# Performance work log

Hardware: AMD Instinct MI355X
Metric: run time of the kernel (lower is better)

Reference implementation:

```python
import jax, jax.numpy as jnp
import numpy as np

C_EM, H_EM, C_A = 256, 8, 32
S, R = 1024, 256
LN_EPS = 1e-5
MASK_BIAS = 1e9


def setup_inputs() -> dict:
    key = jax.random.key(0)
    ks = jax.random.split(key, 8)
    sc = 0.02
    m = jax.random.normal(ks[0], (S, R, C_EM), jnp.float32)
    # binary column mask (float mask in the original; int here so it is a constant)
    mask = (jax.random.uniform(ks[1], (S, R)) < 0.9).astype(jnp.int32)
    return {
        "m": m,
        "ln_g": jnp.ones((C_EM,), jnp.float32),
        "ln_b": jnp.zeros((C_EM,), jnp.float32),
        "w_q": jax.random.normal(ks[2], (C_EM, H_EM, C_A), jnp.float32) * sc,
        "w_k": jax.random.normal(ks[3], (C_EM, C_A), jnp.float32) * sc,
        "w_v": jax.random.normal(ks[4], (C_EM, C_A), jnp.float32) * sc,
        "w_g": jax.random.normal(ks[5], (C_EM, H_EM, C_A), jnp.float32) * sc,
        "b_g": jnp.zeros((H_EM, C_A), jnp.float32),
        "w_o": jax.random.normal(ks[6], (H_EM, C_A, C_EM), jnp.float32) * sc,
        "b_o": jnp.zeros((C_EM,), jnp.float32),
        "mask": mask,
    }


def reference(m, ln_g, ln_b, w_q, w_k, w_v, w_g, b_g, w_o, b_o, mask):
    maskf = mask.astype(m.dtype)  # [s, r]
    # LayerNorm over c_em (biased variance, eps=1e-5, torch default)
    mu = jnp.mean(m, axis=-1, keepdims=True)
    var = jnp.mean((m - mu) ** 2, axis=-1, keepdims=True)
    x = (m - mu) * jax.lax.rsqrt(var + LN_EPS) * ln_g + ln_b  # [s, r, c]
    # masked mean-pool over s -> per-column query
    q_pool = jnp.sum(x * maskf[..., None], axis=-3) / (jnp.sum(maskf, axis=-2)[..., None] + 1e-10)  # [r, c]
    Q = jnp.einsum('rc,chd->rhd', q_pool, w_q) * (1.0 / np.sqrt(C_A))  # [r, h, d]
    K = jnp.einsum('src,cd->srd', x, w_k)  # [s, r, d]
    V = jnp.einsum('src,cd->srd', x, w_v)  # [s, r, d]
    G = jax.nn.sigmoid(jnp.einsum('src,chd->srhd', x, w_g) + b_g)  # [s, r, h, d]
    bias = (maskf - 1.0) * MASK_BIAS  # [s, r]
    logits = jnp.einsum('rhd,srd->srh', Q, K) + bias[..., None]  # [s, r, h]
    A = jax.nn.softmax(logits, axis=-3)  # softmax over s
    O = jnp.einsum('srh,srd->rhd', A, V)  # [r, h, d]
    out = jnp.einsum('srhd,hdc->src', O[None, :, :, :] * G, w_o) + b_o  # [s, r, c]
    return out
```

## Files before the change

### kernel.cpp

```cpp
#include <hip/hip_runtime.h>
#include <math.h>

#define S_DIM 1024
#define R_DIM 256
#define C_DIM 256
#define SCALE 0.17677669529663687f

typedef short bf16x8 __attribute__((ext_vector_type(8)));
typedef float f32x4 __attribute__((ext_vector_type(4)));

__device__ __forceinline__ float wred(float v) {
#pragma unroll
  for (int m = 32; m >= 1; m >>= 1) v += __shfl_xor(v, m, 64);
  return v;
}

__device__ __forceinline__ short f2bf(float f) {
  union { float f; unsigned u; } v;
  v.f = f;
  unsigned r = v.u + 0x7fffu + ((v.u >> 16) & 1u);
  return (short)(r >> 16);
}

__device__ __forceinline__ float bf2f(short s) {
  union { unsigned u; float f; } v;
  v.u = ((unsigned)(unsigned short)s) << 16;
  return v.f;
}

__device__ __forceinline__ float fast_sigmoid_mul(float o, float gl) {
  return o * __builtin_amdgcn_rcpf(1.f + __expf(-gl));
}

__global__ __launch_bounds__(256)
void k0_prep(const float* __restrict__ w_g, const float* __restrict__ w_o,
             const float* __restrict__ w_k, const float* __restrict__ w_v,
             short* __restrict__ wgB, short* __restrict__ woB,
             short* __restrict__ wkvB) {
  const int id = blockIdx.x * 256 + threadIdx.x;
  if (id < 16384) {
    const int which = id >> 13;
    const int s = id & 8191;
    const int n = s & 255, g = (s >> 8) & 3, kb = s >> 10;
    const float* W = which ? w_o : w_g;
    short* Out = which ? woB : wgB;
#pragma unroll
    for (int j = 0; j < 8; ++j)
      Out[(((size_t)kb * 256 + n) * 4 + g) * 8 + j] =
          f2bf(W[(size_t)(kb * 32 + g * 8 + j) * 256 + n]);
  } else {
    const int s = id - 16384;
    const int n = s & 63, g = (s >> 6) & 3, kb = s >> 8;
    const float* W = (n < 32) ? w_k : w_v;
    const int nn = n & 31;
#pragma unroll
    for (int j = 0; j < 8; ++j)
      wkvB[(((size_t)kb * 64 + n) * 4 + g) * 8 + j] =
          f2bf(W[(size_t)(kb * 32 + g * 8 + j) * 32 + nn]);
  }
}

__global__ __launch_bounds__(256, 3)
void k1_ln_kv(const float* __restrict__ mIn, const float* __restrict__ ln_g,
              const float* __restrict__ ln_b, const short* __restrict__ wkvB,
              const int* __restrict__ mask,
              float* __restrict__ mu_ws, float* __restrict__ rs_ws,
              float* __restrict__ K_ws, float* __restrict__ V_ws,
              float* __restrict__ pool_ws) {
  __shared__ __align__(16) short A_lds[2048 * 8];
  __shared__ float mask_s[64];
  __shared__ float4 poolp[4][64];
  const int r  = blockIdx.y;
  const int s0 = blockIdx.x * 64;
  const int t  = threadIdx.x;

  if (t < 64) mask_s[t] = mask[(s0 + t) * R_DIM + r] ? 1.f : 0.f;

  {
    const int rw = t >> 2;
    const int q  = t & 3;
    const size_t p = (size_t)(s0 + rw) * R_DIM + r;
    const float* src = mIn + p * C_DIM + q * 64;
    float4 xv[16];
    float sum = 0.f, ssq = 0.f;
#pragma unroll
    for (int i = 0; i < 16; ++i) {
      xv[i] = *(const float4*)(src + i * 4);
      sum += xv[i].x + xv[i].y + xv[i].z + xv[i].w;
      ssq += xv[i].x * xv[i].x + xv[i].y * xv[i].y + xv[i].z * xv[i].z +
             xv[i].w * xv[i].w;
    }
    sum += __shfl_xor(sum, 1, 64); ssq += __shfl_xor(ssq, 1, 64);
    sum += __shfl_xor(sum, 2, 64); ssq += __shfl_xor(ssq, 2, 64);
    const float mu = sum * (1.f / 256.f);
    const float var = ssq * (1.f / 256.f) - mu * mu;
    const float rs = rsqrtf(var + 1e-5f);
    if (q == 0) { mu_ws[p] = mu; rs_ws[p] = rs; }

    const int gw = rw >> 4;
    const int lf0 = rw & 15;
#pragma unroll
    for (int kh = 0; kh < 2; ++kh) {
      const int kb = 2 * q + kh;
#pragma unroll
      for (int g = 0; g < 4; ++g) {
        const int lidx = kh * 32 + g * 8;
        const float4 a0 = xv[lidx >> 2], a1 = xv[(lidx >> 2) + 1];
        const float4 g0 = *(const float4*)(ln_g + kb * 32 + g * 8);
        const float4 g1 = *(const float4*)(ln_g + kb * 32 + g * 8 + 4);
        const float4 b0 = *(const float4*)(ln_b + kb * 32 + g * 8);
        const float4 b1 = *(const float4*)(ln_b + kb * 32 + g * 8 + 4);
        bf16x8 f;
        f[0] = f2bf((a0.x - mu) * rs * g0.x + b0.x);
        f[1] = f2bf((a0.y - mu) * rs * g0.y + b0.y);
        f[2] = f2bf((a0.z - mu) * rs * g0.z + b0.z);
        f[3] = f2bf((a0.w - mu) * rs * g0.w + b0.w);
        f[4] = f2bf((a1.x - mu) * rs * g1.x + b1.x);
        f[5] = f2bf((a1.y - mu) * rs * g1.y + b1.y);
        f[6] = f2bf((a1.z - mu) * rs * g1.z + b1.z);
        f[7] = f2bf((a1.w - mu) * rs * g1.w + b1.w);
        int byte = (((gw * 8 + kb) * 64 + lf0 + g * 16) << 4) ^ (((kb >> 1) & 3) << 5);
        *(bf16x8*)((char*)A_lds + byte) = f;
      }
    }
  }
  __syncthreads();

  {
    const int w = t >> 6, l = t & 63;
    const int lm = l & 15, g = l >> 4;
    f32x4 acc[4];
#pragma unroll
    for (int ni = 0; ni < 4; ++ni) acc[ni] = (f32x4){0.f, 0.f, 0.f, 0.f};
#pragma unroll
    for (int kb = 0; kb < 8; ++kb) {
      const int byte = (((w * 8 + kb) * 64 + l) << 4) ^ (((kb >> 1) & 3) << 5);
      const bf16x8 a = *(const bf16x8*)((char*)A_lds + byte);
      bf16x8 bfr[4];
#pragma unroll
      for (int ni = 0; ni < 4; ++ni)
        bfr[ni] = *(const bf16x8*)(wkvB + (((size_t)kb * 64 + lm + ni * 16) * 4 + g) * 8);
#pragma unroll
      for (int ni = 0; ni < 4; ++ni)
        acc[ni] = __builtin_amdgcn_mfma_f32_16x16x32_bf16(a, bfr[ni], acc[ni], 0, 0, 0);
    }
#pragma unroll
    for (int ni = 0; ni < 4; ++ni) {
      const int col = lm + ni * 16;
      float* Out = (col < 32) ? K_ws : V_ws;
      const int cc = col & 31;
#pragma unroll
      for (int reg = 0; reg < 4; ++reg) {
        const int s = s0 + w * 16 + g * 4 + reg;
        Out[((size_t)s * R_DIM + r) * 32 + cc] = acc[ni][reg];
      }
    }
  }

  {
    const int lc = t & 63;
    const int wq = t >> 6;
    const int kb = lc >> 3, g2 = (lc >> 1) & 3, bh = (lc & 1) * 4;
    float4 ps = make_float4(0.f, 0.f, 0.f, 0.f);
    for (int i = 0; i < 16; ++i) {
      const int rloc = (i + lc) & 15;
      const int byte =
          ((((wq * 8 + kb) * 64 + rloc + g2 * 16) << 4) + bh * 2) ^ (((kb >> 1) & 3) << 5);
      const short4 xb = *(const short4*)((char*)A_lds + byte);
      const float mk = mask_s[wq * 16 + rloc];
      ps.x += mk * bf2f(xb.x);
      ps.y += mk * bf2f(xb.y);
      ps.z += mk * bf2f(xb.z);
      ps.w += mk * bf2f(xb.w);
    }
    poolp[wq][lc] = ps;
  }
  __syncthreads();
  if (t < 64) {
    const float4 a = poolp[0][t], b = poolp[1][t], c = poolp[2][t], d = poolp[3][t];
    atomicAdd(&pool_ws[r * C_DIM + t * 4 + 0], a.x + b.x + c.x + d.x);
    atomicAdd(&pool_ws[r * C_DIM + t * 4 + 1], a.y + b.y + c.y + d.y);
    atomicAdd(&pool_ws[r * C_DIM + t * 4 + 2], a.z + b.z + c.z + d.z);
    atomicAdd(&pool_ws[r * C_DIM + t * 4 + 3], a.w + b.w + c.w + d.w);
  }
}

__global__ __launch_bounds__(256, 2)
void k3_attn(const float* __restrict__ K_ws, const float* __restrict__ V_ws,
             const int* __restrict__ mask, const float* __restrict__ pool_ws,
             const float* __restrict__ w_q, float* __restrict__ O_ws) {
  __shared__ float q[256];
  __shared__ float qp[256];
  __shared__ float lg[1024 * 9];
  __shared__ float kv[256 * 36];
  __shared__ float mh[8], inv[8];
  __shared__ float wsum[4];
  const int r = blockIdx.x, t = threadIdx.x;

  int mk[4];
#pragma unroll
  for (int ch = 0; ch < 4; ++ch) mk[ch] = mask[(ch * 256 + t) * R_DIM + r];
  float cf = wred((float)(mk[0] + mk[1] + mk[2] + mk[3]));
  if ((t & 63) == 0) wsum[t >> 6] = cf;
  __syncthreads();
  const float denom = wsum[0] + wsum[1] + wsum[2] + wsum[3] + 1e-10f;
  qp[t] = pool_ws[r * C_DIM + t] / denom;
  __syncthreads();
  {
    float qa = 0.f;
    for (int c = 0; c < 256; ++c) qa += qp[c] * w_q[c * 256 + t];
    q[t] = qa * SCALE;
  }
  __syncthreads();

  for (int ch = 0; ch < 4; ++ch) {
    const int sb = ch * 256;
    __syncthreads();
    for (int f = t; f < 2048; f += 256) {
      const int sl = f >> 3, dq = f & 7;
      *(float4*)(kv + sl * 36 + dq * 4) =
          *(const float4*)(K_ws + ((size_t)(sb + sl) * R_DIM + r) * 32 + dq * 4);
    }
    __syncthreads();
    float kr[32];
#pragma unroll
    for (int dq = 0; dq < 8; ++dq)
      *(float4*)(kr + dq * 4) = *(float4*)(kv + t * 36 + dq * 4);
    const float bias = mk[ch] ? 0.f : -1e9f;
#pragma unroll
    for (int h = 0; h < 8; ++h) {
      float a = 0.f;
#pragma unroll
      for (int d = 0; d < 32; ++d) a += q[h * 32 + d] * kr[d];
      lg[(sb + t) * 9 + h] = a + bias;
    }
  }
  __syncthreads();
  {
    const int h = t >> 5, l32 = t & 31;
    float mx = -INFINITY;
    for (int k = 0; k < 32; ++k) mx = fmaxf(mx, lg[(l32 + 32 * k) * 9 + h]);
#pragma unroll
    for (int mkk = 16; mkk >= 1; mkk >>= 1) mx = fmaxf(mx, __shfl_xor(mx, mkk, 64));
    float sm = 0.f;
    for (int k = 0; k < 32; ++k) sm += __expf(lg[(l32 + 32 * k) * 9 + h] - mx);
#pragma unroll
    for (int mkk = 16; mkk >= 1; mkk >>= 1) sm += __shfl_xor(sm, mkk, 64);
    if (l32 == 0) { mh[h] = mx; inv[h] = 1.f / sm; }
  }
  __syncthreads();
  for (int f = t; f < 8192; f += 256) {
    const int s = f >> 3, h = f & 7;
    lg[s * 9 + h] = __expf(lg[s * 9 + h] - mh[h]) * inv[h];
  }
  const int h = t >> 5, d = t & 31;
  float o = 0.f;
  for (int ch = 0; ch < 4; ++ch) {
    const int sb = ch * 256;
    __syncthreads();
    for (int f = t; f < 2048; f += 256) {
      const int sl = f >> 3, dq = f & 7;
      *(float4*)(kv + sl * 36 + dq * 4) =
          *(const float4*)(V_ws + ((size_t)(sb + sl) * R_DIM + r) * 32 + dq * 4);
    }
    __syncthreads();
    for (int sl = 0; sl < 256; ++sl)
      o += lg[(sb + sl) * 9 + h] * kv[sl * 36 + d];
  }
  O_ws[r * 256 + t] = o;
}

__global__ __launch_bounds__(256, 4)
void k4_mfma(const float* __restrict__ mIn, const float* __restrict__ ln_g,
             const float* __restrict__ ln_b, const float* __restrict__ mu_ws,
             const float* __restrict__ rs_ws, const short* __restrict__ wgB,
             const float* __restrict__ b_g, const float* __restrict__ O_ws,
             const short* __restrict__ woB, const float* __restrict__ b_o,
             float* __restrict__ out) {
  __shared__ __align__(16) short A_lds[2048 * 8];
  const int t = threadIdx.x;
  const int p0 = blockIdx.x * 64;
  const int r0 = p0 & 255;
  const int l = t & 63;
  const int w = t >> 6;
  const int lm = l & 15;
  const int g = l >> 4;
  const int col = w * 64 + lm;

  bf16x8 bb_c[4], bb_n[4];
#pragma unroll
  for (int ni = 0; ni < 4; ++ni)
    bb_c[ni] = *(const bf16x8*)(wgB + (((size_t)0 * 256 + col + ni * 16) * 4 + g) * 8);

  {
    const int row = w * 16 + lm;
    const size_t p = (size_t)(p0 + row);
    const float mu = mu_ws[p], rs = rs_ws[p];
    const float* mrow = mIn + p * 256 + g * 8;
    const float* gp = ln_g + g * 8;
    const float* bp = ln_b + g * 8;
#pragma unroll
    for (int kb = 0; kb < 8; ++kb) {
      const float4 m0 = *(const float4*)(mrow + kb * 32);
      const float4 m1 = *(const float4*)(mrow + kb * 32 + 4);
      const float4 g0 = *(const float4*)(gp + kb * 32);
      const float4 g1 = *(const float4*)(gp + kb * 32 + 4);
      const float4 b0 = *(const float4*)(bp + kb * 32);
      const float4 b1 = *(const float4*)(bp + kb * 32 + 4);
      bf16x8 xf;
      xf[0] = f2bf((m0.x - mu) * rs * g0.x + b0.x);
      xf[1] = f2bf((m0.y - mu) * rs * g0.y + b0.y);
      xf[2] = f2bf((m0.z - mu) * rs * g0.z + b0.z);
      xf[3] = f2bf((m0.w - mu) * rs * g0.w + b0.w);
      xf[4] = f2bf((m1.x - mu) * rs * g1.x + b1.x);
      xf[5] = f2bf((m1.y - mu) * rs * g1.y + b1.y);
      xf[6] = f2bf((m1.z - mu) * rs * g1.z + b1.z);
      xf[7] = f2bf((m1.w - mu) * rs * g1.w + b1.w);
      *(bf16x8*)(A_lds + ((w * 8 + kb) * 64 + l) * 8) = xf;
    }
  }
  __syncthreads();

  f32x4 acc[4][4];

#pragma unroll
  for (int ni = 0; ni < 4; ++ni) {
    const float bg = b_g[col + ni * 16];
#pragma unroll
    for (int mi = 0; mi < 4; ++mi) acc[mi][ni] = (f32x4){bg, bg, bg, bg};
  }
#pragma unroll
  for (int kb = 0; kb < 8; ++kb) {
    bf16x8 a[4];
#pragma unroll
    for (int mi = 0; mi < 4; ++mi)
      a[mi] = *(const bf16x8*)(A_lds + ((mi * 8 + kb) * 64 + l) * 8);
    if (kb < 7) {
#pragma unroll
      for (int ni = 0; ni < 4; ++ni)
        bb_n[ni] = *(const bf16x8*)(wgB +
            (((size_t)(kb + 1) * 256 + col + ni * 16) * 4 + g) * 8);
    }
#pragma unroll
    for (int mi = 0; mi < 4; ++mi)
#pragma unroll
      for (int ni = 0; ni < 4; ++ni)
        acc[mi][ni] = __builtin_amdgcn_mfma_f32_16x16x32_bf16(a[mi], bb_c[ni], acc[mi][ni], 0, 0, 0);
#pragma unroll
    for (int ni = 0; ni < 4; ++ni) bb_c[ni] = bb_n[ni];
  }

#pragma unroll
  for (int ni = 0; ni < 4; ++ni)
    bb_c[ni] = *(const bf16x8*)(woB + (((size_t)0 * 256 + col + ni * 16) * 4 + g) * 8);
  __syncthreads();

#pragma unroll
  for (int mi = 0; mi < 4; ++mi) {
#pragma unroll
    for (int ni = 0; ni < 4; ++ni) {
      const int c2 = col + ni * 16;
      const int kb2 = c2 >> 5, g2 = (c2 >> 3) & 3, b2 = c2 & 7;
#pragma unroll
      for (int reg = 0; reg < 4; ++reg) {
        const int row = mi * 16 + g * 4 + reg;
        const float o = O_ws[(r0 + row) * 256 + c2];
        const float tv = fast_sigmoid_mul(o, acc[mi][ni][reg]);
        const int u = (mi * 8 + kb2) * 64 + (g * 4 + reg) + g2 * 16;
        const int byte = ((u << 4) ^ (((u >> 4) & 3) << 4)) + b2 * 2;
        *(short*)((char*)A_lds + byte) = f2bf(tv);
      }
    }
  }
  __syncthreads();

#pragma unroll
  for (int ni = 0; ni < 4; ++ni) {
    const float bo = b_o[col + ni * 16];
#pragma unroll
    for (int mi = 0; mi < 4; ++mi) acc[mi][ni] = (f32x4){bo, bo, bo, bo};
  }
#pragma unroll
  for (int kb = 0; kb < 8; ++kb) {
    bf16x8 a[4];
#pragma unroll
    for (int mi = 0; mi < 4; ++mi) {
      const int u = (mi * 8 + kb) * 64 + l;
      a[mi] = *(const bf16x8*)((char*)A_lds + ((u << 4) ^ (g << 4)));
    }
    if (kb < 7) {
#pragma unroll
      for (int ni = 0; ni < 4; ++ni)
        bb_n[ni] = *(const bf16x8*)(woB +
            (((size_t)(kb + 1) * 256 + col + ni * 16) * 4 + g) * 8);
    }
#pragma unroll
    for (int mi = 0; mi < 4; ++mi)
#pragma unroll
      for (int ni = 0; ni < 4; ++ni)
        acc[mi][ni] = __builtin_amdgcn_mfma_f32_16x16x32_bf16(a[mi], bb_c[ni], acc[mi][ni], 0, 0, 0);
#pragma unroll
    for (int ni = 0; ni < 4; ++ni) bb_c[ni] = bb_n[ni];
  }

#pragma unroll
  for (int mi = 0; mi < 4; ++mi)
#pragma unroll
    for (int ni = 0; ni < 4; ++ni)
#pragma unroll
      for (int reg = 0; reg < 4; ++reg) {
        const int row = mi * 16 + g * 4 + reg;
        out[(size_t)(p0 + row) * 256 + col + ni * 16] = acc[mi][ni][reg];
      }
}

extern "C" void kernel_launch(void* const* d_in, const int* in_sizes, int n_in,
                              void* d_out, int out_size, void* d_ws, size_t ws_size,
                              hipStream_t stream) {
  const float* mIn  = (const float*)d_in[0];
  const float* ln_g = (const float*)d_in[1];
  const float* ln_b = (const float*)d_in[2];
  const float* w_q  = (const float*)d_in[3];
  const float* w_k  = (const float*)d_in[4];
  const float* w_v  = (const float*)d_in[5];
  const float* w_g  = (const float*)d_in[6];
  const float* b_g  = (const float*)d_in[7];
  const float* w_o  = (const float*)d_in[8];
  const float* b_o  = (const float*)d_in[9];
  const int*   mask = (const int*)d_in[10];
  float* outp = (float*)d_out;

  char* ws = (char*)d_ws;
  const size_t NP = (size_t)S_DIM * R_DIM;
  float* mu_ws   = (float*)ws;
  float* rs_ws   = mu_ws + NP;
  float* K_ws    = rs_ws + NP;
  float* V_ws    = K_ws + NP * 32;
  float* pool_ws = V_ws + NP * 32;
  float* O_ws    = pool_ws + 65536;
  short* wgB     = (short*)(O_ws + 65536);
  short* woB     = wgB + 65536;
  short* wkvB    = woB + 65536;

  hipMemsetAsync(pool_ws, 0, 65536 * sizeof(float), stream);

  k0_prep<<<72, 256, 0, stream>>>(w_g, w_o, w_k, w_v, wgB, woB, wkvB);
  k1_ln_kv<<<dim3(S_DIM / 64, R_DIM), 256, 0, stream>>>(
      mIn, ln_g, ln_b, wkvB, mask, mu_ws, rs_ws, K_ws, V_ws, pool_ws);
  k3_attn<<<R_DIM, 256, 0, stream>>>(K_ws, V_ws, mask, pool_ws, w_q, O_ws);
  k4_mfma<<<dim3(S_DIM * R_DIM / 64), 256, 0, stream>>>(
      mIn, ln_g, ln_b, mu_ws, rs_ws, wgB, b_g, O_ws, woB, b_o, outp);
}
```

Before: 395.9 us.

## Process two 64-row tiles per block with double-buffered LDS software pipeline

The final fused gate/output GEMM kernel now handles two 64-row tiles per block, using two LDS buffers. Loads of the second tile's input rows overlap the first tile's gate GEMM, and the scatter and second GEMM stages of the two tiles are interleaved. This is meant to hide global-load latency and barrier stalls behind MFMA work. In exchange it doubles LDS use, raises register pressure (16 float4 prefetch registers), halves the grid and lowers the occupancy target to 2 blocks per CU. It also drops the previous B-fragment register prefetch.

```diff
diff --git a/kernel.cpp b/kernel.cpp
--- a/kernel.cpp
+++ b/kernel.cpp
@@ -270,148 +270,196 @@
   O_ws[r * 256 + t] = o;
 }
 
-__global__ __launch_bounds__(256, 4)
+#define K4_WRITEX(L, MU, RS)                                                \
+  {                                                                         \
+    const float* gp_ = ln_g + g * 8;                                        \
+    const float* bp_ = ln_b + g * 8;                                        \
+    _Pragma("unroll")                                                       \
+    for (int kb = 0; kb < 8; ++kb) {                                        \
+      const float4 g0 = *(const float4*)(gp_ + kb * 32);                    \
+      const float4 g1 = *(const float4*)(gp_ + kb * 32 + 4);                \
+      const float4 b0 = *(const float4*)(bp_ + kb * 32);                    \
+      const float4 b1 = *(const float4*)(bp_ + kb * 32 + 4);                \
+      const float4 m0 = mv[2 * kb], m1 = mv[2 * kb + 1];                    \
+      bf16x8 xf;                                                            \
+      xf[0] = f2bf((m0.x - (MU)) * (RS) * g0.x + b0.x);                     \
+      xf[1] = f2bf((m0.y - (MU)) * (RS) * g0.y + b0.y);                     \
+      xf[2] = f2bf((m0.z - (MU)) * (RS) * g0.z + b0.z);                     \
+      xf[3] = f2bf((m0.w - (MU)) * (RS) * g0.w + b0.w);                     \
+      xf[4] = f2bf((m1.x - (MU)) * (RS) * g1.x + b1.x);                     \
+      xf[5] = f2bf((m1.y - (MU)) * (RS) * g1.y + b1.y);                     \
+      xf[6] = f2bf((m1.z - (MU)) * (RS) * g1.z + b1.z);                     \
+      xf[7] = f2bf((m1.w - (MU)) * (RS) * g1.w + b1.w);                     \
+      *(bf16x8*)((L) + ((w * 8 + kb) * 64 + l) * 8) = xf;                   \
+    }                                                                       \
+  }
+
+#define K4_G1(L)                                                            \
+  {                                                                         \
+    _Pragma("unroll")                                                       \
+    for (int ni = 0; ni < 4; ++ni) {                                        \
+      const float bg = b_g[col + ni * 16];                                  \
+      _Pragma("unroll")                                                     \
+      for (int mi = 0; mi < 4; ++mi) acc[mi][ni] = (f32x4){bg, bg, bg, bg}; \
+    }                                                                       \
+    _Pragma("unroll")                                                       \
+    for (int kb = 0; kb < 8; ++kb) {                                        \
+      bf16x8 bb[4], a[4];                                                   \
+      _Pragma("unroll")                                                     \
+      for (int ni = 0; ni < 4; ++ni)                                        \
+        bb[ni] = *(const bf16x8*)(wgB +                                     \
+            (((size_t)kb * 256 + col + ni * 16) * 4 + g) * 8);              \
+      _Pragma("unroll")                                                     \
+      for (int mi = 0; mi < 4; ++mi)                                        \
+        a[mi] = *(const bf16x8*)((L) + ((mi * 8 + kb) * 64 + l) * 8);       \
+      _Pragma("unroll")                                                     \
+      for (int mi = 0; mi < 4; ++mi)                                        \
+        _Pragma("unroll")                                                   \
+        for (int ni = 0; ni < 4; ++ni)                                      \
+          acc[mi][ni] = __builtin_amdgcn_mfma_f32_16x16x32_bf16(            \
+              a[mi], bb[ni], acc[mi][ni], 0, 0, 0);                         \
+    }                                                                       \
+  }
+
+#define K4_SCAT(L, R0)                                                      \
+  {                                                                         \
+    _Pragma("unroll")                                                       \
+    for (int mi = 0; mi < 4; ++mi) {                                        \
+      _Pragma("unroll")                                                     \
+      for (int ni = 0; ni < 4; ++ni) {                                      \
+        const int c2 = col + ni * 16;                                       \
+        const int kb2 = c2 >> 5, g2 = (c2 >> 3) & 3, b2 = c2 & 7;           \
+        _Pragma("unroll")                                                   \
+        for (int reg = 0; reg < 4; ++reg) {                                 \
+          const int rw2 = mi * 16 + g * 4 + reg;                            \
+          const float o = O_ws[((R0) + rw2) * 256 + c2];                    \
+          const float tv = fast_sigmoid_mul(o, acc[mi][ni][reg]);           \
+          const int u = (mi * 8 + kb2) * 64 + (g * 4 + reg) + g2 * 16;      \
+          const int byte = ((u << 4) ^ (((u >> 4) & 3) << 4)) + b2 * 2;     \
+          *(short*)((char*)(L) + byte) = f2bf(tv);                          \
+        }                                                                   \
+      }                                                                     \
+    }                                                                       \
+  }
+
+#define K4_G2(L)                                                            \
+  {                                                                         \
+    _Pragma("unroll")                                                       \
+    for (int ni = 0; ni < 4; ++ni) {                                        \
+      const float bo = b_o[col + ni * 16];                                  \
+      _Pragma("unroll")                                                     \
+      for (int mi = 0; mi < 4; ++mi) acc[mi][ni] = (f32x4){bo, bo, bo, bo}; \
+    }                                                                       \
+    _Pragma("unroll")                                                       \
+    for (int kb = 0; kb < 8; ++kb) {                                        \
+      bf16x8 bb[4], a[4];                                                   \
+      _Pragma("unroll")                                                     \
+      for (int ni = 0; ni < 4; ++ni)                                        \
+        bb[ni] = *(const bf16x8*)(woB +                                     \
+            (((size_t)kb * 256 + col + ni * 16) * 4 + g) * 8);              \
+      _Pragma("unroll")                                                     \
+      for (int mi = 0; mi < 4; ++mi) {                                      \
+        const int u = (mi * 8 + kb) * 64 + l;                               \
+        a[mi] = *(const bf16x8*)((char*)(L) + ((u << 4) ^ (g << 4)));       \
+      }                                                                     \
+      _Pragma("unroll")                                                     \
+      for (int mi = 0; mi < 4; ++mi)                                        \
+        _Pragma("unroll")                                                   \
+        for (int ni = 0; ni < 4; ++ni)                                      \
+          acc[mi][ni] = __builtin_amdgcn_mfma_f32_16x16x32_bf16(            \
+              a[mi], bb[ni], acc[mi][ni], 0, 0, 0);                         \
+    }                                                                       \
+  }
+
+#define K4_STORE(PBASE)                                                     \
+  _Pragma("unroll")                                                         \
+  for (int mi = 0; mi < 4; ++mi)                                            \
+    _Pragma("unroll")                                                       \
+    for (int ni = 0; ni < 4; ++ni)                                          \
+      _Pragma("unroll")                                                     \
+      for (int reg = 0; reg < 4; ++reg) {                                   \
+        const int rw2 = mi * 16 + g * 4 + reg;                              \
+        out[(size_t)((PBASE) + rw2) * 256 + col + ni * 16] =                \
+            acc[mi][ni][reg];                                               \
+      }
+
+__global__ __launch_bounds__(256, 2)
 void k4_mfma(const float* __restrict__ mIn, const float* __restrict__ ln_g,
              const float* __restrict__ ln_b, const float* __restrict__ mu_ws,
              const float* __restrict__ rs_ws, const short* __restrict__ wgB,
              const float* __restrict__ b_g, const float* __restrict__ O_ws,
              const short* __restrict__ woB, const float* __restrict__ b_o,
              float* __restrict__ out) {
-  __shared__ __align__(16) short A_lds[2048 * 8];
+  __shared__ __align__(16) short L0[2048 * 8];
+  __shared__ __align__(16) short L1[2048 * 8];
   const int t = threadIdx.x;
-  const int p0 = blockIdx.x * 64;
-  const int r0 = p0 & 255;
-  const int l = t & 63;
-  const int w = t >> 6;
-  const int lm = l & 15;
-  const int g = l >> 4;
+  const int l = t & 63, w = t >> 6, lm = l & 15, g = l >> 4;
+  const int pA = blockIdx.x * 128;
+  const int r0A = pA & 255;
+  const int r0B = r0A + 64;
   const int col = w * 64 + lm;
-
-  bf16x8 bb_c[4], bb_n[4];
-#pragma unroll
-  for (int ni = 0; ni < 4; ++ni)
-    bb_c[ni] = *(const bf16x8*)(wgB + (((size_t)0 * 256 + col + ni * 16) * 4 + g) * 8);
-
-  {
-    const int row = w * 16 + lm;
-    const size_t p = (size_t)(p0 + row);
-    const float mu = mu_ws[p], rs = rs_ws[p];
+  const int srow = w * 16 + lm;
+
+  float4 mv[16];
+  f32x4 acc[4][4];
+
+  {
+    const size_t p = (size_t)(pA + srow);
+    const float mu0 = mu_ws[p], rs0 = rs_ws[p];
     const float* mrow = mIn + p * 256 + g * 8;
-    const float* gp = ln_g + g * 8;
-    const float* bp = ln_b + g * 8;
 #pragma unroll
     for (int kb = 0; kb < 8; ++kb) {
-      const float4 m0 = *(const float4*)(mrow + kb * 32);
-      const float4 m1 = *(const float4*)(mrow + kb * 32 + 4);
-      const float4 g0 = *(const float4*)(gp + kb * 32);
-      const float4 g1 = *(const float4*)(gp + kb * 32 + 4);
-      const float4 b0 = *(const float4*)(bp + kb * 32);
-      const float4 b1 = *(const float4*)(bp + kb * 32 + 4);
-      bf16x8 xf;
-      xf[0] = f2bf((m0.x - mu) * rs * g0.x + b0.x);
-      xf[1] = f2bf((m0.y - mu) * rs * g0.y + b0.y);
-      xf[2] = f2bf((m0.z - mu) * rs * g0.z + b0.z);
-      xf[3] = f2bf((m0.w - mu) * rs * g0.w + b0.w);
-      xf[4] = f2bf((m1.x - mu) * rs * g1.x + b1.x);
-      xf[5] = f2bf((m1.y - mu) * rs * g1.y + b1.y);
-      xf[6] = f2bf((m1.z - mu) * rs * g1.z + b1.z);
-      xf[7] = f2bf((m1.w - mu) * rs * g1.w + b1.w);
-      *(bf16x8*)(A_lds + ((w * 8 + kb) * 64 + l) * 8) = xf;
-    }
-  }
-  __syncthreads();
-
-  f32x4 acc[4][4];
-
-#pragma unroll
-  for (int ni = 0; ni < 4; ++ni) {
-    const float bg = b_g[col + ni * 16];
-#pragma unroll
-    for (int mi = 0; mi < 4; ++mi) acc[mi][ni] = (f32x4){bg, bg, bg, bg};
-  }
-#pragma unroll
-  for (int kb = 0; kb < 8; ++kb) {
-    bf16x8 a[4];
-#pragma unroll
-    for (int mi = 0; mi < 4; ++mi)
-      a[mi] = *(const bf16x8*)(A_lds + ((mi * 8 + kb) * 64 + l) * 8);
-    if (kb < 7) {
+      mv[2 * kb]     = *(const float4*)(mrow + kb * 32);
+      mv[2 * kb + 1] = *(const float4*)(mrow + kb * 32 + 4);
+    }
+    K4_WRITEX(L0, mu0, rs0)
+  }
+  __syncthreads();
+
+  {
+    const size_t pB = (size_t)(pA + 64 + srow);
+    const float mu1 = mu_ws[pB], rs1 = rs_ws[pB];
+    const float* mrowB = mIn + pB * 256 + g * 8;
+#pragma unroll
+    for (int ni = 0; ni < 4; ++ni) {
+      const float bg = b_g[col + ni * 16];
+#pragma unroll
+      for (int mi = 0; mi < 4; ++mi) acc[mi][ni] = (f32x4){bg, bg, bg, bg};
+    }
+#pragma unroll
+    for (int kb = 0; kb < 8; ++kb) {
+      bf16x8 bb[4], a[4];
 #pragma unroll
       for (int ni = 0; ni < 4; ++ni)
-        bb_n[ni] = *(const bf16x8*)(wgB +
-            (((size_t)(kb + 1) * 256 + col + ni * 16) * 4 + g) * 8);
-    }
-#pragma unroll
-    for (int mi = 0; mi < 4; ++mi)
-#pragma unroll
-      for (int ni = 0; ni < 4; ++ni)
-        acc[mi][ni] = __builtin_amdgcn_mfma_f32_16x16x32_bf16(a[mi], bb_c[ni], acc[mi][ni], 0, 0, 0);
-#pragma unroll
-    for (int ni = 0; ni < 4; ++ni) bb_c[ni] = bb_n[ni];
-  }
-
-#pragma unroll
-  for (int ni = 0; ni < 4; ++ni)
-    bb_c[ni] = *(const bf16x8*)(woB + (((size_t)0 * 256 + col + ni * 16) * 4 + g) * 8);
-  __syncthreads();
-
-#pragma unroll
-  for (int mi = 0; mi < 4; ++mi) {
-#pragma unroll
-    for (int ni = 0; ni < 4; ++ni) {
-      const int c2 = col + ni * 16;
-      const int kb2 = c2 >> 5, g2 = (c2 >> 3) & 3, b2 = c2 & 7;
-#pragma unroll
-      for (int reg = 0; reg < 4; ++reg) {
-        const int row = mi * 16 + g * 4 + reg;
-        const float o = O_ws[(r0 + row) * 256 + c2];
-        const float tv = fast_sigmoid_mul(o, acc[mi][ni][reg]);
-        const int u = (mi * 8 + kb2) * 64 + (g * 4 + reg) + g2 * 16;
-        const int byte = ((u << 4) ^ (((u >> 4) & 3) << 4)) + b2 * 2;
-        *(short*)((char*)A_lds + byte) = f2bf(tv);
-      }
-    }
-  }
-  __syncthreads();
-
-#pragma unroll
-  for (int ni = 0; ni < 4; ++ni) {
-    const float bo = b_o[col + ni * 16];
-#pragma unroll
-    for (int mi = 0; mi < 4; ++mi) acc[mi][ni] = (f32x4){bo, bo, bo, bo};
-  }
-#pragma unroll
-  for (int kb = 0; kb < 8; ++kb) {
-    bf16x8 a[4];
-#pragma unroll
-    for (int mi = 0; mi < 4; ++mi) {
-      const int u = (mi * 8 + kb) * 64 + l;
-      a[mi] = *(const bf16x8*)((char*)A_lds + ((u << 4) ^ (g << 4)));
-    }
-    if (kb < 7) {
-#pragma unroll
-      for (int ni = 0; ni < 4; ++ni)
-        bb_n[ni] = *(const bf16x8*)(woB +
-            (((size_t)(kb + 1) * 256 + col + ni * 16) * 4 + g) * 8);
-    }
-#pragma unroll
-    for (int mi = 0; mi < 4; ++mi)
-#pragma unroll
-      for (int ni = 0; ni < 4; ++ni)
-        acc[mi][ni] = __builtin_amdgcn_mfma_f32_16x16x32_bf16(a[mi], bb_c[ni], acc[mi][ni], 0, 0, 0);
-#pragma unroll
-    for (int ni = 0; ni < 4; ++ni) bb_c[ni] = bb_n[ni];
-  }
-
-#pragma unroll
-  for (int mi = 0; mi < 4; ++mi)
-#pragma unroll
-    for (int ni = 0; ni < 4; ++ni)
-#pragma unroll
-      for (int reg = 0; reg < 4; ++reg) {
-        const int row = mi * 16 + g * 4 + reg;
-        out[(size_t)(p0 + row) * 256 + col + ni * 16] = acc[mi][ni][reg];
-      }
+        bb[ni] = *(const bf16x8*)(wgB +
+            (((size_t)kb * 256 + col + ni * 16) * 4 + g) * 8);
+      mv[2 * kb]     = *(const float4*)(mrowB + kb * 32);
+      mv[2 * kb + 1] = *(const float4*)(mrowB + kb * 32 + 4);
+#pragma unroll
+      for (int mi = 0; mi < 4; ++mi)
+        a[mi] = *(const bf16x8*)(L0 + ((mi * 8 + kb) * 64 + l) * 8);
+#pragma unroll
+      for (int mi = 0; mi < 4; ++mi)
+#pragma unroll
+        for (int ni = 0; ni < 4; ++ni)
+          acc[mi][ni] = __builtin_amdgcn_mfma_f32_16x16x32_bf16(
+              a[mi], bb[ni], acc[mi][ni], 0, 0, 0);
+    }
+    K4_WRITEX(L1, mu1, rs1)
+  }
+  __syncthreads();
+
+  K4_SCAT(L0, r0A)
+  K4_G1(L1)
+  __syncthreads();
+
+  K4_SCAT(L1, r0B)
+  K4_G2(L0)
+  K4_STORE(pA)
+  __syncthreads();
+
+  K4_G2(L1)
+  K4_STORE(pA + 64)
 }
 
 extern "C" void kernel_launch(void* const* d_in, const int* in_sizes, int n_in,
@@ -448,6 +496,6 @@
   k1_ln_kv<<<dim3(S_DIM / 64, R_DIM), 256, 0, stream>>>(
       mIn, ln_g, ln_b, wkvB, mask, mu_ws, rs_ws, K_ws, V_ws, pool_ws);
   k3_attn<<<R_DIM, 256, 0, stream>>>(K_ws, V_ws, mask, pool_ws, w_q, O_ws);
-  k4_mfma<<<dim3(S_DIM * R_DIM / 64), 256, 0, stream>>>(
+  k4_mfma<<<dim3(S_DIM * R_DIM / 128), 256, 0, stream>>>(
       mIn, ln_g, ln_b, mu_ws, rs_ws, wgB, b_g, O_ws, woB, b_o, outp);
 }
```

New measurement: 398.1 us. No clear change (+0.6%).
